# Kernel optimization log

Hardware: AMD Instinct MI355X
Metric: run time of the kernel (lower is better)

Reference implementation:

```python
import jax, jax.numpy as jnp
import numpy as np

N_SITES = 1024
HIDDEN = 64
BATCH = 16384  # num_samples


def setup_inputs() -> dict:
    key = jax.random.key(0)
    ks = jax.random.split(key, 7)
    H = HIDDEN
    s = 0.1  # weight init scale
    return {
        "u": jax.random.uniform(ks[0], (BATCH, N_SITES), jnp.float32),  # bernoulli noise
        "w_ih": jax.random.normal(ks[1], (3 * H, 1), jnp.float32) * s,   # gate order [r,z,n]
        "w_hh": jax.random.normal(ks[2], (3 * H, H), jnp.float32) * s,
        "b_ih": jax.random.normal(ks[3], (3 * H,), jnp.float32) * s,
        "b_hh": jax.random.normal(ks[4], (3 * H,), jnp.float32) * s,
        "head_w": jax.random.normal(ks[5], (1, H), jnp.float32) * s,
        "head_b": jax.random.normal(ks[6], (1,), jnp.float32) * s,
    }


def reference(u, w_ih, w_hh, b_ih, b_hh, head_w, head_b):
    # sequential over sites via lax.scan. PyTorch GRU cell math, gates [r,z,n].
    H = w_hh.shape[1]
    B = u.shape[0]
    w_ih_vec = w_ih[:, 0]  # input_size == 1 -> [3H]

    def step(carry, u_t):
        h, prev = carry  # h: [B,H], prev: [B] previous sampled bit
        gx = prev[:, None] * w_ih_vec[None, :] + b_ih  # [B,3H]
        gh = h @ w_hh.T + b_hh                          # [B,3H]
        r = jax.nn.sigmoid(gx[:, :H] + gh[:, :H])
        z = jax.nn.sigmoid(gx[:, H:2 * H] + gh[:, H:2 * H])
        n = jnp.tanh(gx[:, 2 * H:] + r * gh[:, 2 * H:])
        h_new = (1.0 - z) * n + z * h
        logit = h_new @ head_w[0] + head_b[0]  # [B]
        p = jax.nn.sigmoid(logit)
        bit = (u_t < p).astype(h.dtype)  # bernoulli(p) via pre-drawn uniform
        return (h_new, bit), bit

    h0 = jnp.zeros((B, H), u.dtype)
    prev0 = jnp.zeros((B,), u.dtype)  # torch starts with prev = 0
    _, bits = jax.lax.scan(step, (h0, prev0), u.T)  # bits: [n_sites, B]
    return bits.T.astype(jnp.int32)  # [B, n_sites], matches samples.long()
```

## Files before the change

### kernel.cpp

```cpp
#include <hip/hip_runtime.h>

#define NS 1024
#define NH 64
#define NB 16384

typedef float f32x2 __attribute__((ext_vector_type(2)));
typedef float f32x4 __attribute__((ext_vector_type(4)));

#pragma clang fp contract(off)

#define PKFMA_LO(acc, h, w)                                                  \
  asm("v_pk_fma_f32 %0, %1, %2, %0 op_sel:[0,0,0] op_sel_hi:[1,0,1]"         \
      : "+v"(acc) : "v"(h), "v"(w))
#define PKFMA_HI(acc, h, w)                                                  \
  asm("v_pk_fma_f32 %0, %1, %2, %0 op_sel:[0,1,0] op_sel_hi:[1,1,1]"         \
      : "+v"(acc) : "v"(h), "v"(w))


__device__ __forceinline__ f32x2 xexp2v(f32x2 x) {
  x = __builtin_elementwise_min(x, f32x2{88.3762626647950f, 88.3762626647950f});
  x = __builtin_elementwise_max(x, f32x2{-88.3762626647949f, -88.3762626647949f});
  f32x2 fx = __builtin_elementwise_floor(x * 1.44269504088896341f + 0.5f);
  x = x - fx * 0.693359375f;
  x = x - fx * (-2.12194440e-4f);
  f32x2 z = x * x;
  f32x2 y = {1.9875691500e-4f, 1.9875691500e-4f};
  y = y * x + 1.3981999507e-3f;
  y = y * x + 8.3334519073e-3f;
  y = y * x + 4.1665795894e-2f;
  y = y * x + 1.6666665459e-1f;
  y = y * x + 5.0000001201e-1f;
  y = y * z + x;
  y = y + 1.0f;
  int n0 = (int)fx.x, n1 = (int)fx.y;
  float p0 = __int_as_float((n0 + 127) << 23);
  float p1 = __int_as_float((n1 + 127) << 23);
  f32x2 r;
  r.x = __fmul_rn(y.x, p0);
  r.y = __fmul_rn(y.y, p1);
  return r;
}

__device__ __forceinline__ f32x2 xsigmoid2(f32x2 x) {
  f32x2 e = xexp2v(-x);
  f32x2 d = e + 1.0f;
  f32x2 r;
  r.x = __fdiv_rn(1.0f, d.x);
  r.y = __fdiv_rn(1.0f, d.y);
  return r;
}

__device__ __forceinline__ f32x2 xtanh2(f32x2 x) {
  f32x2 xc = __builtin_elementwise_min(
      __builtin_elementwise_max(x, f32x2{-7.90531110763549805f, -7.90531110763549805f}),
      f32x2{7.90531110763549805f, 7.90531110763549805f});
  f32x2 s = xc * xc;
  f32x2 p = {-2.76076847742355e-16f, -2.76076847742355e-16f};
  p = p * s + 2.00018790482477e-13f;
  p = p * s + (-8.60467152213735e-11f);
  p = p * s + 5.12229709037114e-08f;
  p = p * s + 1.48572235717979e-05f;
  p = p * s + 6.37261928875436e-04f;
  p = p * s + 4.89352455891786e-03f;
  f32x2 num = xc * p;
  f32x2 q = {1.19825839466702e-06f, 1.19825839466702e-06f};
  q = q * s + 1.18534705686654e-04f;
  q = q * s + 2.26843463243900e-03f;
  q = q * s + 4.89352518554385e-03f;
  f32x2 rat;
  rat.x = __fdiv_rn(num.x, q.x);
  rat.y = __fdiv_rn(num.y, q.y);
  f32x2 r;
  r.x = (fabsf(x.x) < 0.0004f) ? x.x : rat.x;
  r.y = (fabsf(x.y) < 0.0004f) ? x.y : rat.y;
  return r;
}

__device__ __forceinline__ float rdlane(float v, int l) {
  return __int_as_float(__builtin_amdgcn_readlane(__float_as_int(v), l));
}

__global__ __launch_bounds__(256, 2) void gru_sample_kernel(
    const float* __restrict__ u, const float* __restrict__ w_ih,
    const float* __restrict__ w_hh, const float* __restrict__ b_ih,
    const float* __restrict__ b_hh, const float* __restrict__ head_w,
    const float* __restrict__ head_b, int* __restrict__ out) {
  const int lane = threadIdx.x & 63;
  const int wv = threadIdx.x >> 6;
  const int rowA = blockIdx.x * 8 + wv * 2;
  const int rowB = rowA + 1;

  __shared__ f32x4 wzn[32][NH];
  __shared__ f32x2 hp[4][NH];

  for (int idx = threadIdx.x; idx < 32 * NH; idx += 256) {
    int kk = idx & 31, j = idx >> 5;
    const float* wzrow = w_hh + (size_t)(64 + j) * NH;
    const float* wnrow = w_hh + (size_t)(128 + j) * NH;
    wzn[kk][j] = f32x4{wzrow[2 * kk], wnrow[2 * kk], wzrow[2 * kk + 1], wnrow[2 * kk + 1]};
  }
  f32x2 wr2[32];
#pragma unroll
  for (int i = 0; i < 32; ++i)
    wr2[i] = *(const f32x2*)&w_hh[(size_t)lane * NH + 2 * i];

  const float bih_r = b_ih[lane], bih_z = b_ih[64 + lane], bih_n = b_ih[128 + lane];
  const float bhh_r = b_hh[lane], bhh_z = b_hh[64 + lane], bhh_n = b_hh[128 + lane];
  const float sum_r = __fadd_rn(w_ih[lane], bih_r);
  const float sum_z = __fadd_rn(w_ih[64 + lane], bih_z);
  const float sum_n = __fadd_rn(w_ih[128 + lane], bih_n);
  const float hwv = head_w[lane];
  const f32x2 hw2 = {hwv, hwv};
  const float hb = head_b[0];
  __syncthreads();

  const float* urA = u + (size_t)rowA * NS;
  const float* urB = u + (size_t)rowB * NS;
  int* orA = out + (size_t)rowA * NS;
  int* orB = out + (size_t)rowB * NS;

  f32x2 h2 = {0.0f, 0.0f};
  int prevA = 0, prevB = 0;
  hp[wv][lane] = h2;
  const f32x4* hp4 = (const f32x4*)&hp[wv][0];

  for (int c = 0; c < 16; ++c) {
    float uA = urA[c * 64 + lane];
    float uB = urB[c * 64 + lane];
    int mybitA = 0, mybitB = 0;
    for (int tt = 0; tt < 64; ++tt) {
      f32x2 ar2 = {0.0f, 0.0f}, az2 = {0.0f, 0.0f}, an2 = {0.0f, 0.0f};
#pragma unroll
      for (int kk = 0; kk < 32; ++kk) {
        f32x4 h4 = hp4[kk];
        f32x4 w4 = wzn[kk][lane];
        f32x2 h2a = __builtin_shufflevector(h4, h4, 0, 1);
        f32x2 h2b = __builtin_shufflevector(h4, h4, 2, 3);
        f32x2 wa = __builtin_shufflevector(w4, w4, 0, 1);
        f32x2 wb = __builtin_shufflevector(w4, w4, 2, 3);
        PKFMA_LO(ar2, h2a, wr2[kk]);
        PKFMA_LO(az2, h2a, wa);
        PKFMA_HI(an2, h2a, wa);
        PKFMA_HI(ar2, h2b, wr2[kk]);
        PKFMA_LO(az2, h2b, wb);
        PKFMA_HI(an2, h2b, wb);
      }
      f32x2 ghr2 = ar2 + bhh_r;
      f32x2 ghz2 = az2 + bhh_z;
      f32x2 ghn2 = an2 + bhh_n;
      f32x2 gxr2 = {prevA ? sum_r : bih_r, prevB ? sum_r : bih_r};
      f32x2 gxz2 = {prevA ? sum_z : bih_z, prevB ? sum_z : bih_z};
      f32x2 gxn2 = {prevA ? sum_n : bih_n, prevB ? sum_n : bih_n};
      f32x2 r2 = xsigmoid2(gxr2 + ghr2);
      f32x2 z2 = xsigmoid2(gxz2 + ghz2);
      f32x2 n2 = xtanh2(gxn2 + r2 * ghn2);
      f32x2 omz = 1.0f - z2;
      h2 = omz * n2 + z2 * h2;
      hp[wv][lane] = h2;

      f32x2 P2 = h2 * hw2;
      f32x2 t, s2;
      t.x = __shfl(P2.x, lane + 16); t.y = __shfl(P2.y, lane + 16);
      s2 = P2 + t;
      t.x = __shfl(P2.x, lane + 32); t.y = __shfl(P2.y, lane + 32);
      s2 = s2 + t;
      t.x = __shfl(P2.x, lane + 48); t.y = __shfl(P2.y, lane + 48);
      s2 = s2 + t;
      t.x = __shfl(s2.x, lane + 8); t.y = __shfl(s2.y, lane + 8);
      s2 = s2 + t;
      t.x = __shfl(s2.x, lane + 4); t.y = __shfl(s2.y, lane + 4);
      s2 = s2 + t;
      t.x = __shfl(s2.x, lane + 2); t.y = __shfl(s2.y, lane + 2);
      s2 = s2 + t;
      t.x = __shfl(s2.x, lane + 1); t.y = __shfl(s2.y, lane + 1);
      s2 = s2 + t;
      float logitA = __fadd_rn(rdlane(s2.x, 0), hb);
      float logitB = __fadd_rn(rdlane(s2.y, 0), hb);
      f32x2 p2 = xsigmoid2(f32x2{logitA, logitB});

      float uAt = rdlane(uA, tt);
      float uBt = rdlane(uB, tt);
      int bA = (uAt < p2.x) ? 1 : 0;
      int bB = (uBt < p2.y) ? 1 : 0;
      prevA = bA;
      prevB = bB;
      mybitA = (lane == tt) ? bA : mybitA;
      mybitB = (lane == tt) ? bB : mybitB;
    }
    orA[c * 64 + lane] = mybitA;
    orB[c * 64 + lane] = mybitB;
  }
}

extern "C" void kernel_launch(void* const* d_in, const int* in_sizes, int n_in,
                              void* d_out, int out_size, void* d_ws, size_t ws_size,
                              hipStream_t stream) {
  const float* u = (const float*)d_in[0];
  const float* w_ih = (const float*)d_in[1];
  const float* w_hh = (const float*)d_in[2];
  const float* b_ih = (const float*)d_in[3];
  const float* b_hh = (const float*)d_in[4];
  const float* head_w = (const float*)d_in[5];
  const float* head_b = (const float*)d_in[6];
  int* out = (int*)d_out;
  dim3 grid(NB / 8), block(256);
  gru_sample_kernel<<<grid, block, 0, stream>>>(u, w_ih, w_hh, b_ih, b_hh,
                                                head_w, head_b, out);
}
```

Measured before the change: 8.962 ms.

## Interleave four independent row-pair recurrences per wave and use DPP reductions

Each wave now advances four independent pairs of batch rows (eight rows) in an unrolled inner loop instead of one pair, so the serial dependency chain of one recurrence can overlap with the others' LDS loads, FMAs and transcendentals. The grid shrinks fourfold to match. The tail of the head-dot-product reduction also switches from ds_bpermute shuffles to DPP row-shift adds. The cost is more registers per wave and fewer waves across the device (2048 vs 8192), which could leave CUs underused or cause spills.

```diff
diff --git a/kernel.cpp b/kernel.cpp
--- a/kernel.cpp
+++ b/kernel.cpp
@@ -80,6 +80,17 @@
   return __int_as_float(__builtin_amdgcn_readlane(__float_as_int(v), l));
 }
 
+__device__ __forceinline__ float dpp_shl_add(float s, const int ctrl) {
+  int t;
+  switch (ctrl) {
+    case 0x108: t = __builtin_amdgcn_update_dpp(0, __float_as_int(s), 0x108, 0xF, 0xF, true); break;
+    case 0x104: t = __builtin_amdgcn_update_dpp(0, __float_as_int(s), 0x104, 0xF, 0xF, true); break;
+    case 0x102: t = __builtin_amdgcn_update_dpp(0, __float_as_int(s), 0x102, 0xF, 0xF, true); break;
+    default:    t = __builtin_amdgcn_update_dpp(0, __float_as_int(s), 0x101, 0xF, 0xF, true); break;
+  }
+  return __fadd_rn(s, __int_as_float(t));
+}
+
 __global__ __launch_bounds__(256, 2) void gru_sample_kernel(
     const float* __restrict__ u, const float* __restrict__ w_ih,
     const float* __restrict__ w_hh, const float* __restrict__ b_ih,
@@ -87,11 +98,10 @@
     const float* __restrict__ head_b, int* __restrict__ out) {
   const int lane = threadIdx.x & 63;
   const int wv = threadIdx.x >> 6;
-  const int rowA = blockIdx.x * 8 + wv * 2;
-  const int rowB = rowA + 1;
+  const int rowBase = blockIdx.x * 32 + wv * 8;
 
   __shared__ f32x4 wzn[32][NH];
-  __shared__ f32x2 hp[4][NH];
+  __shared__ f32x2 hp[4][4][NH];
 
   for (int idx = threadIdx.x; idx < 32 * NH; idx += 256) {
     int kk = idx & 31, j = idx >> 5;
@@ -114,81 +124,101 @@
   const float hb = head_b[0];
   __syncthreads();
 
-  const float* urA = u + (size_t)rowA * NS;
-  const float* urB = u + (size_t)rowB * NS;
-  int* orA = out + (size_t)rowA * NS;
-  int* orB = out + (size_t)rowB * NS;
-
-  f32x2 h2 = {0.0f, 0.0f};
-  int prevA = 0, prevB = 0;
-  hp[wv][lane] = h2;
-  const f32x4* hp4 = (const f32x4*)&hp[wv][0];
-
+  const float* upA[4];
+  const float* upB[4];
+#pragma unroll
+  for (int p = 0; p < 4; ++p) {
+    upA[p] = u + (size_t)(rowBase + 2 * p) * NS;
+    upB[p] = u + (size_t)(rowBase + 2 * p + 1) * NS;
+  }
+
+  f32x2 h2s[4];
+  int prevA[4], prevB[4];
+#pragma unroll
+  for (int p = 0; p < 4; ++p) {
+    h2s[p] = f32x2{0.0f, 0.0f};
+    prevA[p] = 0;
+    prevB[p] = 0;
+    hp[wv][p][lane] = h2s[p];
+  }
+
+#pragma unroll 1
   for (int c = 0; c < 16; ++c) {
-    float uA = urA[c * 64 + lane];
-    float uB = urB[c * 64 + lane];
-    int mybitA = 0, mybitB = 0;
+    float ucA[4], ucB[4];
+    int mbA[4], mbB[4];
+#pragma unroll
+    for (int p = 0; p < 4; ++p) {
+      ucA[p] = upA[p][c * 64 + lane];
+      ucB[p] = upB[p][c * 64 + lane];
+      mbA[p] = 0;
+      mbB[p] = 0;
+    }
+#pragma unroll 1
     for (int tt = 0; tt < 64; ++tt) {
-      f32x2 ar2 = {0.0f, 0.0f}, az2 = {0.0f, 0.0f}, an2 = {0.0f, 0.0f};
-#pragma unroll
-      for (int kk = 0; kk < 32; ++kk) {
-        f32x4 h4 = hp4[kk];
-        f32x4 w4 = wzn[kk][lane];
-        f32x2 h2a = __builtin_shufflevector(h4, h4, 0, 1);
-        f32x2 h2b = __builtin_shufflevector(h4, h4, 2, 3);
-        f32x2 wa = __builtin_shufflevector(w4, w4, 0, 1);
-        f32x2 wb = __builtin_shufflevector(w4, w4, 2, 3);
-        PKFMA_LO(ar2, h2a, wr2[kk]);
-        PKFMA_LO(az2, h2a, wa);
-        PKFMA_HI(an2, h2a, wa);
-        PKFMA_HI(ar2, h2b, wr2[kk]);
-        PKFMA_LO(az2, h2b, wb);
-        PKFMA_HI(an2, h2b, wb);
+#pragma unroll
+      for (int p = 0; p < 4; ++p) {
+        const f32x4* hp4 = (const f32x4*)&hp[wv][p][0];
+        f32x2 ar2 = {0.0f, 0.0f}, az2 = {0.0f, 0.0f}, an2 = {0.0f, 0.0f};
+#pragma unroll
+        for (int kk = 0; kk < 32; ++kk) {
+          f32x4 h4 = hp4[kk];
+          f32x4 w4 = wzn[kk][lane];
+          f32x2 h2a = __builtin_shufflevector(h4, h4, 0, 1);
+          f32x2 h2b = __builtin_shufflevector(h4, h4, 2, 3);
+          f32x2 wa = __builtin_shufflevector(w4, w4, 0, 1);
+          f32x2 wb = __builtin_shufflevector(w4, w4, 2, 3);
+          PKFMA_LO(ar2, h2a, wr2[kk]);
+          PKFMA_LO(az2, h2a, wa);
+          PKFMA_HI(an2, h2a, wa);
+          PKFMA_HI(ar2, h2b, wr2[kk]);
+          PKFMA_LO(az2, h2b, wb);
+          PKFMA_HI(an2, h2b, wb);
+        }
+        f32x2 ghr2 = ar2 + bhh_r;
+        f32x2 ghz2 = az2 + bhh_z;
+        f32x2 ghn2 = an2 + bhh_n;
+        f32x2 gxr2 = {prevA[p] ? sum_r : bih_r, prevB[p] ? sum_r : bih_r};
+        f32x2 gxz2 = {prevA[p] ? sum_z : bih_z, prevB[p] ? sum_z : bih_z};
+        f32x2 gxn2 = {prevA[p] ? sum_n : bih_n, prevB[p] ? sum_n : bih_n};
+        f32x2 r2 = xsigmoid2(gxr2 + ghr2);
+        f32x2 z2 = xsigmoid2(gxz2 + ghz2);
+        f32x2 n2 = xtanh2(gxn2 + r2 * ghn2);
+        f32x2 omz = 1.0f - z2;
+        f32x2 h2 = omz * n2 + z2 * h2s[p];
+        h2s[p] = h2;
+        hp[wv][p][lane] = h2;
+
+        f32x2 P2 = h2 * hw2;
+        f32x2 t16, t32, t48;
+        t16.x = __shfl(P2.x, lane + 16); t16.y = __shfl(P2.y, lane + 16);
+        t32.x = __shfl(P2.x, lane + 32); t32.y = __shfl(P2.y, lane + 32);
+        t48.x = __shfl(P2.x, lane + 48); t48.y = __shfl(P2.y, lane + 48);
+        f32x2 s2 = P2 + t16;
+        s2 = s2 + t32;
+        s2 = s2 + t48;
+        s2.x = dpp_shl_add(s2.x, 0x108); s2.y = dpp_shl_add(s2.y, 0x108);
+        s2.x = dpp_shl_add(s2.x, 0x104); s2.y = dpp_shl_add(s2.y, 0x104);
+        s2.x = dpp_shl_add(s2.x, 0x102); s2.y = dpp_shl_add(s2.y, 0x102);
+        s2.x = dpp_shl_add(s2.x, 0x101); s2.y = dpp_shl_add(s2.y, 0x101);
+        float logitA = __fadd_rn(rdlane(s2.x, 0), hb);
+        float logitB = __fadd_rn(rdlane(s2.y, 0), hb);
+        f32x2 p2 = xsigmoid2(f32x2{logitA, logitB});
+
+        float uAt = rdlane(ucA[p], tt);
+        float uBt = rdlane(ucB[p], tt);
+        int bA = (uAt < p2.x) ? 1 : 0;
+        int bB = (uBt < p2.y) ? 1 : 0;
+        prevA[p] = bA;
+        prevB[p] = bB;
+        mbA[p] = (lane == tt) ? bA : mbA[p];
+        mbB[p] = (lane == tt) ? bB : mbB[p];
       }
-      f32x2 ghr2 = ar2 + bhh_r;
-      f32x2 ghz2 = az2 + bhh_z;
-      f32x2 ghn2 = an2 + bhh_n;
-      f32x2 gxr2 = {prevA ? sum_r : bih_r, prevB ? sum_r : bih_r};
-      f32x2 gxz2 = {prevA ? sum_z : bih_z, prevB ? sum_z : bih_z};
-      f32x2 gxn2 = {prevA ? sum_n : bih_n, prevB ? sum_n : bih_n};
-      f32x2 r2 = xsigmoid2(gxr2 + ghr2);
-      f32x2 z2 = xsigmoid2(gxz2 + ghz2);
-      f32x2 n2 = xtanh2(gxn2 + r2 * ghn2);
-      f32x2 omz = 1.0f - z2;
-      h2 = omz * n2 + z2 * h2;
-      hp[wv][lane] = h2;
-
-      f32x2 P2 = h2 * hw2;
-      f32x2 t, s2;
-      t.x = __shfl(P2.x, lane + 16); t.y = __shfl(P2.y, lane + 16);
-      s2 = P2 + t;
-      t.x = __shfl(P2.x, lane + 32); t.y = __shfl(P2.y, lane + 32);
-      s2 = s2 + t;
-      t.x = __shfl(P2.x, lane + 48); t.y = __shfl(P2.y, lane + 48);
-      s2 = s2 + t;
-      t.x = __shfl(s2.x, lane + 8); t.y = __shfl(s2.y, lane + 8);
-      s2 = s2 + t;
-      t.x = __shfl(s2.x, lane + 4); t.y = __shfl(s2.y, lane + 4);
-      s2 = s2 + t;
-      t.x = __shfl(s2.x, lane + 2); t.y = __shfl(s2.y, lane + 2);
-      s2 = s2 + t;
-      t.x = __shfl(s2.x, lane + 1); t.y = __shfl(s2.y, lane + 1);
-      s2 = s2 + t;
-      float logitA = __fadd_rn(rdlane(s2.x, 0), hb);
-      float logitB = __fadd_rn(rdlane(s2.y, 0), hb);
-      f32x2 p2 = xsigmoid2(f32x2{logitA, logitB});
-
-      float uAt = rdlane(uA, tt);
-      float uBt = rdlane(uB, tt);
-      int bA = (uAt < p2.x) ? 1 : 0;
-      int bB = (uBt < p2.y) ? 1 : 0;
-      prevA = bA;
-      prevB = bB;
-      mybitA = (lane == tt) ? bA : mybitA;
-      mybitB = (lane == tt) ? bB : mybitB;
     }
-    orA[c * 64 + lane] = mybitA;
-    orB[c * 64 + lane] = mybitB;
+#pragma unroll
+    for (int p = 0; p < 4; ++p) {
+      out[(size_t)(rowBase + 2 * p) * NS + c * 64 + lane] = mbA[p];
+      out[(size_t)(rowBase + 2 * p + 1) * NS + c * 64 + lane] = mbB[p];
+    }
   }
 }
 
@@ -203,7 +233,7 @@
   const float* head_w = (const float*)d_in[5];
   const float* head_b = (const float*)d_in[6];
   int* out = (int*)d_out;
-  dim3 grid(NB / 8), block(256);
+  dim3 grid(NB / 32), block(256);
   gru_sample_kernel<<<grid, block, 0, stream>>>(u, w_ih, w_hh, b_ih, b_hh,
                                                 head_w, head_b, out);
 }
```

New measurement: 9.267 ms. 3.4% more time.
